# Optimization experiments

Hardware: AMD Instinct MI355X
Metric: run time of the kernel (lower is better)

The kernel has to match this reference:

```python
import jax, jax.numpy as jnp
import numpy as np

WEIGHT = 0.1
NEIGHBORHOOD_SIZE = 3
EPSILON = 1e-06


def setup_inputs() -> dict:
    key = jax.random.key(0)
    x = jax.random.normal(key, (8, 3, 1024, 1024), dtype=jnp.float32)
    return {"x": x}


def reference(x):
    b, c, h, w = x.shape
    total = jnp.zeros((), dtype=x.dtype)
    for k in range(-NEIGHBORHOOD_SIZE, NEIGHBORHOOD_SIZE + 1):
        for l in range(-NEIGHBORHOOD_SIZE, NEIGHBORHOOD_SIZE + 1):
            if k == 0 and l == 0:
                continue
            shifted = jnp.roll(x, shift=(k, l), axis=(2, 3))
            diff = jnp.abs(x - shifted)
            total = total + jnp.sqrt(diff * diff + EPSILON).sum()
    return WEIGHT * total / (b * c * h * w)
```

## Files before the change

kernel.cpp:

```cpp
#include <hip/hip_runtime.h>


#define HDIM 1024
#define WDIM 1024
#define PLANES 24
#define MASK 1023
#define NTOT (PLANES * HDIM * WDIM)
#define RROWS 8
#define BLOCKS_PER_PLANE (HDIM / RROWS)
#define NBLOCKS (PLANES * BLOCKS_PER_PLANE)

__device__ __forceinline__ void load_row(const float* __restrict__ rb,
                                         int j, int cl, int cr, float* w) {
    float4 a = *(const float4*)(rb + cl);
    float4 b = *(const float4*)(rb + j);
    float4 c = *(const float4*)(rb + cr);
    w[0] = a.x; w[1] = a.y; w[2]  = a.z; w[3]  = a.w;
    w[4] = b.x; w[5] = b.y; w[6]  = b.z; w[7]  = b.w;
    w[8] = c.x; w[9] = c.y; w[10] = c.z; w[11] = c.w;
}

__global__ __launch_bounds__(256) void btv_main(const float* __restrict__ x,
                                                float* __restrict__ partial) {
    const int plane  = blockIdx.x >> 7;
    const int istart = (blockIdx.x & 127) * RROWS;
    const int j  = threadIdx.x << 2;
    const int cl = (j - 4) & MASK;
    const int cr = (j + 4) & MASK;
    const float* pbase = x + (size_t)plane * (HDIM * WDIM);

    float w[4][12];
#pragma unroll
    for (int k = 0; k < 4; ++k)
        load_row(pbase + (((istart + k) & MASK) * WDIM), j, cl, cr, w[k]);

    float acc0 = 0.f, acc1 = 0.f, acc2 = 0.f, acc3 = 0.f;

#pragma unroll
    for (int r = 0; r < RROWS; ++r) {
        float nxt[12];
        if (r < RROWS - 1)
            load_row(pbase + (((istart + r + 4) & MASK) * WDIM), j, cl, cr, nxt);

        const float* w0 = w[r & 3];
        const float* w1 = w[(r + 1) & 3];
        const float* w2 = w[(r + 2) & 3];
        const float* w3 = w[(r + 3) & 3];

#pragma unroll
        for (int p = 0; p < 4; ++p) {
            const float own = w0[4 + p];
            float a = 0.f;
            a += fabsf(own - w0[5 + p]);
            a += fabsf(own - w0[6 + p]);
            a += fabsf(own - w0[7 + p]);
#pragma unroll
            for (int l = -3; l <= 3; ++l) a += fabsf(own - w1[4 + p + l]);
#pragma unroll
            for (int l = -3; l <= 3; ++l) a += fabsf(own - w2[4 + p + l]);
#pragma unroll
            for (int l = -3; l <= 3; ++l) a += fabsf(own - w3[4 + p + l]);
            if (p == 0) acc0 += a;
            else if (p == 1) acc1 += a;
            else if (p == 2) acc2 += a;
            else acc3 += a;
        }

        if (r < RROWS - 1) {
#pragma unroll
            for (int c = 0; c < 12; ++c) w[r & 3][c] = nxt[c];
        }
    }

    float acc = (acc0 + acc1) + (acc2 + acc3);

#pragma unroll
    for (int off = 32; off > 0; off >>= 1)
        acc += __shfl_down(acc, off, 64);

    __shared__ float s[4];
    const int lane = threadIdx.x & 63;
    const int wid  = threadIdx.x >> 6;
    if (lane == 0) s[wid] = acc;
    __syncthreads();
    if (threadIdx.x == 0)
        partial[blockIdx.x] = (s[0] + s[1]) + (s[2] + s[3]);
}

__global__ __launch_bounds__(256) void btv_fin(const float* __restrict__ partial,
                                               float* __restrict__ out) {
    double s = 0.0;
    for (int i = threadIdx.x; i < NBLOCKS; i += 256)
        s += (double)partial[i];
#pragma unroll
    for (int off = 32; off > 0; off >>= 1)
        s += __shfl_down(s, off, 64);
    __shared__ double sh[4];
    const int lane = threadIdx.x & 63;
    const int wid  = threadIdx.x >> 6;
    if (lane == 0) sh[wid] = s;
    __syncthreads();
    if (threadIdx.x == 0) {
        double t = (sh[0] + sh[1]) + (sh[2] + sh[3]);
        *out = (float)(t * (0.2 / (double)NTOT));
    }
}

extern "C" void kernel_launch(void* const* d_in, const int* in_sizes, int n_in,
                              void* d_out, int out_size, void* d_ws, size_t ws_size,
                              hipStream_t stream) {
    const float* x = (const float*)d_in[0];
    float* out = (float*)d_out;
    float* partial = (float*)d_ws;

    btv_main<<<NBLOCKS, 256, 0, stream>>>(x, partial);
    btv_fin<<<1, 256, 0, stream>>>(partial, out);
}
```

Before: 147.6 us.

## Stage rows through double-buffered LDS instead of triple global halo loads

Each thread now loads a single float4 per row from global memory, writes it into a double-buffered LDS row with wrap-around halo padding, and reads the left/center/right windows back from LDS. Previously every row was fetched three times from global memory (left, center, right float4s). The next row's global load is issued one iteration early to hide latency. In exchange it adds a block-wide __syncthreads per row and LDS traffic. The two-slot buffer may also be overwritten while other waves are still reading it.

```diff
diff --git a/kernel.cpp b/kernel.cpp
--- a/kernel.cpp
+++ b/kernel.cpp
@@ -9,38 +9,61 @@
 #define RROWS 8
 #define BLOCKS_PER_PLANE (HDIM / RROWS)
 #define NBLOCKS (PLANES * BLOCKS_PER_PLANE)
-
-__device__ __forceinline__ void load_row(const float* __restrict__ rb,
-                                         int j, int cl, int cr, float* w) {
-    float4 a = *(const float4*)(rb + cl);
-    float4 b = *(const float4*)(rb + j);
-    float4 c = *(const float4*)(rb + cr);
-    w[0] = a.x; w[1] = a.y; w[2]  = a.z; w[3]  = a.w;
-    w[4] = b.x; w[5] = b.y; w[6]  = b.z; w[7]  = b.w;
-    w[8] = c.x; w[9] = c.y; w[10] = c.z; w[11] = c.w;
-}
+#define LROW 1032
 
 __global__ __launch_bounds__(256) void btv_main(const float* __restrict__ x,
                                                 float* __restrict__ partial) {
+    __shared__ float lds[2 * LROW];
     const int plane  = blockIdx.x >> 7;
     const int istart = (blockIdx.x & 127) * RROWS;
     const int j  = threadIdx.x << 2;
-    const int cl = (j - 4) & MASK;
-    const int cr = (j + 4) & MASK;
     const float* pbase = x + (size_t)plane * (HDIM * WDIM);
+
+    float4 g[4];
+#pragma unroll
+    for (int k = 0; k < 4; ++k)
+        g[k] = *(const float4*)(pbase + ((istart + k) & MASK) * WDIM + j);
 
     float w[4][12];
 #pragma unroll
-    for (int k = 0; k < 4; ++k)
-        load_row(pbase + (((istart + k) & MASK) * WDIM), j, cl, cr, w[k]);
+    for (int k = 0; k < 4; ++k) {
+        float* slot = lds + (k & 1) * LROW;
+        *(float4*)(slot + 4 + j) = g[k];
+        if (j == 0)        *(float4*)(slot + 4 + WDIM) = g[k];
+        if (j == WDIM - 4) *(float4*)(slot)            = g[k];
+        __syncthreads();
+        float4 a = *(const float4*)(slot + j);
+        float4 b = *(const float4*)(slot + j + 4);
+        float4 c = *(const float4*)(slot + j + 8);
+        w[k][0] = a.x; w[k][1] = a.y; w[k][2]  = a.z; w[k][3]  = a.w;
+        w[k][4] = b.x; w[k][5] = b.y; w[k][6]  = b.z; w[k][7]  = b.w;
+        w[k][8] = c.x; w[k][9] = c.y; w[k][10] = c.z; w[k][11] = c.w;
+    }
+
+    float4 gc = *(const float4*)(pbase + ((istart + 4) & MASK) * WDIM + j);
 
     float acc0 = 0.f, acc1 = 0.f, acc2 = 0.f, acc3 = 0.f;
 
 #pragma unroll
     for (int r = 0; r < RROWS; ++r) {
+        float4 gn;
+        if (r < RROWS - 2)
+            gn = *(const float4*)(pbase + ((istart + r + 5) & MASK) * WDIM + j);
+
         float nxt[12];
-        if (r < RROWS - 1)
-            load_row(pbase + (((istart + r + 4) & MASK) * WDIM), j, cl, cr, nxt);
+        if (r < RROWS - 1) {
+            float* slot = lds + (r & 1) * LROW;
+            *(float4*)(slot + 4 + j) = gc;
+            if (j == 0)        *(float4*)(slot + 4 + WDIM) = gc;
+            if (j == WDIM - 4) *(float4*)(slot)            = gc;
+            __syncthreads();
+            float4 a = *(const float4*)(slot + j);
+            float4 b = *(const float4*)(slot + j + 4);
+            float4 c = *(const float4*)(slot + j + 8);
+            nxt[0] = a.x; nxt[1] = a.y; nxt[2]  = a.z; nxt[3]  = a.w;
+            nxt[4] = b.x; nxt[5] = b.y; nxt[6]  = b.z; nxt[7]  = b.w;
+            nxt[8] = c.x; nxt[9] = c.y; nxt[10] = c.z; nxt[11] = c.w;
+        }
 
         const float* w0 = w[r & 3];
         const float* w1 = w[(r + 1) & 3];
@@ -69,6 +92,7 @@
         if (r < RROWS - 1) {
 #pragma unroll
             for (int c = 0; c < 12; ++c) w[r & 3][c] = nxt[c];
+            gc = gn;
         }
     }
 
```

Result: slower. 263.2 us (+78.3%).
